# Kernel tuning notes

Hardware: AMD Instinct MI355X
Metric: run time of the kernel (lower is better)

## Reference

```python
import jax, jax.numpy as jnp
import numpy as np

N_NODES = 10000
N_EDGES = 80000
N_GRAPHS = 64
H, D = 4, 512          # num_heads, out_feats
EMB = 768
HFEAT = 512
NCLS = 2
SLOPE = 0.2            # DGL GATConv default negative_slope
BN_EPS = 1e-5


def setup_inputs() -> dict:
    key = jax.random.key(0)
    ks = jax.random.split(key, 24)
    f32 = jnp.float32
    rn = lambda k, s, sc=0.02: jax.random.normal(k, s, dtype=f32) * sc
    inp = {
        "node_feat": jax.random.normal(ks[0], (N_NODES, EMB), dtype=f32),
        "func_feat": jax.random.normal(ks[1], (N_NODES, EMB), dtype=f32),
        "W1": rn(ks[2], (EMB, H * D)),
        "al1": rn(ks[3], (H, D), 0.1),
        "ar1": rn(ks[4], (H, D), 0.1),
        "b1": jnp.zeros((H * D,), f32),
        "W2": rn(ks[5], (H * D, H * D)),
        "al2": rn(ks[6], (H, D), 0.1),
        "ar2": rn(ks[7], (H, D), 0.1),
        "b2": jnp.zeros((H * D,), f32),
        "Wfc": rn(ks[8], (H * D, HFEAT)),
        "bfc": jnp.zeros((HFEAT,), f32),
        "Wfco": rn(ks[9], (EMB, HFEAT)),
        "bfco": jnp.zeros((HFEAT,), f32),
        "Wh": rn(ks[10], (8, HFEAT, HFEAT)),
        "bh": jnp.zeros((8, HFEAT), f32),
        "gamma": jnp.ones((HFEAT,), f32),
        "beta": jnp.zeros((HFEAT,), f32),
        "Whfc": rn(ks[11], (HFEAT, HFEAT)),
        "bhfc": jnp.zeros((HFEAT,), f32),
        "Wf": rn(ks[12], (HFEAT, NCLS)),
        "bf": jnp.zeros((NCLS,), f32),
        "src": jax.random.randint(ks[13], (N_EDGES,), 0, N_NODES),
        "dst": jax.random.randint(ks[14], (N_EDGES,), 0, N_NODES),
        "graph_id": jnp.sort(jax.random.randint(ks[15], (N_NODES,), 0, N_GRAPHS)),
    }
    return inp


def gat_conv(h, W, al, ar, b, src, dst):
    """DGL GATConv (eval mode): fc -> per-head attention logits -> edge
    softmax over incoming edges -> scatter-sum -> +bias. Returns (N, H*D)."""
    feat = (h @ W).reshape(-1, H, D)                      # (N,H,D)
    el = jnp.einsum('nhd,hd->nh', feat, al)               # (N,H)
    er = jnp.einsum('nhd,hd->nh', feat, ar)
    e = jax.nn.leaky_relu(el[src] + er[dst], SLOPE)       # (E,H)
    emax = jax.ops.segment_max(e, dst, num_segments=N_NODES)
    ex = jnp.exp(e - emax[dst])
    den = jax.ops.segment_sum(ex, dst, num_segments=N_NODES)
    a = ex / den[dst]                                     # edge softmax (E,H)
    msg = feat[src] * a[:, :, None]                       # (E,H,D) gather+weight
    out = jax.ops.segment_sum(msg, dst, num_segments=N_NODES)
    return (out + b.reshape(1, H, D)).reshape(-1, H * D)


def reference(node_feat, func_feat, W1, al1, ar1, b1, W2, al2, ar2, b2,
              Wfc, bfc, Wfco, bfco, Wh, bh, gamma, beta, Whfc, bhfc,
              Wf, bf, src, dst, graph_id):
    h = gat_conv(node_feat, W1, al1, ar1, b1, src, dst)   # (N, 2048)
    h = gat_conv(h, W2, al2, ar2, b2, src, dst)           # (N, 2048)
    h = jax.nn.elu(h @ Wfc + bfc)                         # (N, 512)
    h_func = jax.nn.elu(func_feat @ Wfco + bfco)          # (N, 512)
    for i in range(8):
        h = jax.nn.elu(h @ Wh[i] + bh[i])
        h_func = jax.nn.elu(h_func @ Wh[i] + bh[i])       # dead for output (as in torch)
    counts = jax.ops.segment_sum(jnp.ones((N_NODES,), h.dtype), graph_id,
                                 num_segments=N_GRAPHS)
    hg = jax.ops.segment_sum(h, graph_id, num_segments=N_GRAPHS)
    hg = hg / jnp.maximum(counts, 1.0)[:, None]           # dgl.mean_nodes (G, 512)
    # BatchNorm1d eval with running_mean=0, running_var=1
    hg = hg / jnp.sqrt(1.0 + BN_EPS) * gamma + beta
    hg = jax.nn.elu(hg @ Whfc + bhfc)
    return hg @ Wf + bf                                   # (G, NCLS)
```

## Files before the change

### kernel.cpp

```cpp
#include <hip/hip_runtime.h>
#include <hip/hip_bf16.h>
#include <math.h>

#define N_NODES 10000
#define N_EDGES 80000
#define N_GRAPHS 64
#define NH 4
#define HD 512
#define HDTOT 2048
#define EMB 768
#define HFEAT 512

typedef _Float16 half8 __attribute__((ext_vector_type(8)));
typedef _Float16 half4 __attribute__((ext_vector_type(4)));
typedef float f32x4 __attribute__((ext_vector_type(4)));

__device__ __forceinline__ void gload_lds16(const void* g, void* l) {
  __builtin_amdgcn_global_load_lds(
      (const __attribute__((address_space(1))) unsigned int*)g,
      (__attribute__((address_space(3))) unsigned int*)l, 16, 0, 0);
}

template <int BM>
__global__ __launch_bounds__(256) void gemm_f16_kernel(
    const _Float16* __restrict__ A, const _Float16* __restrict__ BT,
    const float* __restrict__ bias, _Float16* __restrict__ C,
    int M, int N, int K, int act) {
  constexpr int WR = (BM == 128) ? 2 : 1;
  constexpr int WC = 4 / WR;
  constexpr int MI = (BM / WR) / 16;
  constexpr int NI = (128 / WC) / 16;
  constexpr int NW = NI * 16;
  constexpr int CS = NW + 4;
  constexpr int GPR = NW / 8;

  __shared__ _Float16 smem[(BM + 128) * 32];
  _Float16* As = smem;
  _Float16* Bs = smem + BM * 32;

  const int bn = blockIdx.x * 128, bm = blockIdx.y * BM;
  const int t = threadIdx.x;
  const int lane = t & 63, wave = t >> 6;
  const int wr = wave / WC, wc = wave % WC;
  const int m0 = wr * (BM / WR), n0 = wc * NW;
  const int fr = lane & 15, fq = lane >> 4;

  f32x4 acc[MI][NI];
#pragma unroll
  for (int i = 0; i < MI; ++i)
#pragma unroll
    for (int j = 0; j < NI; ++j) acc[i][j] = (f32x4){0.f, 0.f, 0.f, 0.f};

  for (int k0 = 0; k0 < K; k0 += 32) {
    __syncthreads();
#pragma unroll
    for (int it = 0; it < BM / 64; ++it) {
      int gid = it * 256 + t;
      int r = gid >> 2;
      int q = (gid & 3) ^ ((r >> 1) & 3);
      int grow = bm + r;
      if (grow >= M) grow = M - 1;
      gload_lds16(A + (size_t)grow * K + k0 + q * 8,
                  &As[(it * 256 + wave * 64) * 8]);
    }
#pragma unroll
    for (int it = 0; it < 2; ++it) {
      int gid = it * 256 + t;
      int r = gid >> 2;
      int q = (gid & 3) ^ ((r >> 1) & 3);
      gload_lds16(BT + (size_t)(bn + r) * K + k0 + q * 8,
                  &Bs[(it * 256 + wave * 64) * 8]);
    }
    __syncthreads();

    half8 af[MI], bf[NI];
#pragma unroll
    for (int mi = 0; mi < MI; ++mi) {
      int m = m0 + mi * 16 + fr;
      af[mi] = *(const half8*)&As[m * 32 + (fq ^ ((m >> 1) & 3)) * 8];
    }
#pragma unroll
    for (int ni = 0; ni < NI; ++ni) {
      int n = n0 + ni * 16 + fr;
      bf[ni] = *(const half8*)&Bs[n * 32 + (fq ^ ((n >> 1) & 3)) * 8];
    }
#pragma unroll
    for (int mi = 0; mi < MI; ++mi)
#pragma unroll
      for (int ni = 0; ni < NI; ++ni)
        acc[mi][ni] = __builtin_amdgcn_mfma_f32_16x16x32_f16(
            af[mi], bf[ni], acc[mi][ni], 0, 0, 0);
  }
  __syncthreads();
  _Float16* cs = smem + wave * 16 * CS;
#pragma unroll
  for (int mi = 0; mi < MI; ++mi) {
#pragma unroll
    for (int ni = 0; ni < NI; ++ni) {
      float bb = bias ? bias[bn + n0 + ni * 16 + fr] : 0.f;
#pragma unroll
      for (int j = 0; j < 4; ++j) {
        float v = acc[mi][ni][j] + bb;
        if (act == 1) v = v > 0.f ? v : expm1f(v);
        cs[(fq * 4 + j) * CS + ni * 16 + fr] = (_Float16)v;
      }
    }
#pragma unroll
    for (int i = 0; i < NW / 32; ++i) {
      int piece = i * 64 + lane;
      int r = piece / GPR, g = piece % GPR;
      int grow = bm + m0 + mi * 16 + r;
      if (grow < M) {
        half8 v = *(const half8*)&cs[r * CS + g * 8];
        *(half8*)&C[(size_t)grow * N + bn + n0 + g * 8] = v;
      }
    }
  }
}

__global__ __launch_bounds__(256) void convert_wt_kernel(
    const float* __restrict__ W, _Float16* __restrict__ WT, int K, int N) {
  __shared__ float tile[32][33];
  W += (size_t)blockIdx.z * K * N;
  WT += (size_t)blockIdx.z * K * N;
  int k0 = blockIdx.x * 32, n0 = blockIdx.y * 32;
  int t = threadIdx.x;
  int r = t >> 3, c4 = (t & 7) * 4;
  float4 v = *(const float4*)(W + (size_t)(k0 + r) * N + n0 + c4);
  tile[r][c4 + 0] = v.x;
  tile[r][c4 + 1] = v.y;
  tile[r][c4 + 2] = v.z;
  tile[r][c4 + 3] = v.w;
  __syncthreads();
  float x0 = tile[c4 + 0][r], x1 = tile[c4 + 1][r];
  float x2 = tile[c4 + 2][r], x3 = tile[c4 + 3][r];
  size_t o = (size_t)(n0 + r) * K + k0 + c4;
  *(half4*)&WT[o] = (half4){(_Float16)x0, (_Float16)x1, (_Float16)x2, (_Float16)x3};
}

__global__ void convert_f32_f16_kernel(const float* __restrict__ x,
                                       _Float16* __restrict__ y, int n4) {
  int gid = blockIdx.x * blockDim.x + threadIdx.x;
  if (gid >= n4) return;
  float4 v = *(const float4*)(x + gid * 4);
  *(half4*)(y + gid * 4) =
      (half4){(_Float16)v.x, (_Float16)v.y, (_Float16)v.z, (_Float16)v.w};
}

__global__ void hist_kernel(const int* __restrict__ dst, int* __restrict__ cnt, int E) {
  int gid = blockIdx.x * blockDim.x + threadIdx.x;
  if (gid < E) atomicAdd(&cnt[dst[gid]], 1);
}

__global__ void scan_kernel(const int* __restrict__ cnt, int* __restrict__ row_ptr,
                            int* __restrict__ cursor, int n) {
  __shared__ int part[256];
  int t = threadIdx.x;
  int chunk = (n + 255) / 256;
  int s0 = t * chunk;
  int s1 = min(s0 + chunk, n);
  int sum = 0;
  for (int i = s0; i < s1; ++i) sum += cnt[i];
  part[t] = sum;
  __syncthreads();
  if (t == 0) {
    int acc = 0;
    for (int i = 0; i < 256; ++i) { int v = part[i]; part[i] = acc; acc += v; }
    row_ptr[n] = acc;
  }
  __syncthreads();
  int run = part[t];
  for (int i = s0; i < s1; ++i) {
    row_ptr[i] = run;
    cursor[i] = run;
    run += cnt[i];
  }
}

__global__ void scatter_kernel(const int* __restrict__ src, const int* __restrict__ dst,
                               int* __restrict__ cursor, int* __restrict__ csr_src,
                               int* __restrict__ csr_dst, int E) {
  int gid = blockIdx.x * blockDim.x + threadIdx.x;
  if (gid < E) {
    int d = dst[gid];
    int pos = atomicAdd(&cursor[d], 1);
    csr_src[pos] = src[gid];
    csr_dst[pos] = d;
  }
}

__global__ __launch_bounds__(256) void el_er_kernel(
    const _Float16* __restrict__ feat, const float* __restrict__ al,
    const float* __restrict__ ar, float* __restrict__ el, float* __restrict__ er) {
  int n = blockIdx.x;
  int t = threadIdx.x;
  int h = t >> 6, lane = t & 63;
  half8 f = *(const half8*)(feat + (size_t)n * HDTOT + h * HD + lane * 8);
  const float* ap = al + h * HD + lane * 8;
  const float* rp = ar + h * HD + lane * 8;
  float4 a0 = *(const float4*)ap, a1 = *(const float4*)(ap + 4);
  float4 r0 = *(const float4*)rp, r1 = *(const float4*)(rp + 4);
  float f0 = (float)f[0], f1 = (float)f[1], f2 = (float)f[2], f3 = (float)f[3];
  float f4 = (float)f[4], f5 = (float)f[5], f6 = (float)f[6], f7 = (float)f[7];
  float sl = f0 * a0.x + f1 * a0.y + f2 * a0.z + f3 * a0.w +
             f4 * a1.x + f5 * a1.y + f6 * a1.z + f7 * a1.w;
  float sr = f0 * r0.x + f1 * r0.y + f2 * r0.z + f3 * r0.w +
             f4 * r1.x + f5 * r1.y + f6 * r1.z + f7 * r1.w;
  for (int off = 32; off; off >>= 1) {
    sl += __shfl_down(sl, off);
    sr += __shfl_down(sr, off);
  }
  if (lane == 0) {
    el[n * NH + h] = sl;
    er[n * NH + h] = sr;
  }
}

__global__ void edge_e_kernel(const float* __restrict__ el, const float* __restrict__ er,
                              const int* __restrict__ csr_src,
                              const int* __restrict__ csr_dst,
                              float* __restrict__ e_buf, int EH) {
  int gid = blockIdx.x * blockDim.x + threadIdx.x;
  if (gid >= EH) return;
  int p = gid >> 2, h = gid & 3;
  float v = el[csr_src[p] * NH + h] + er[csr_dst[p] * NH + h];
  e_buf[gid] = v >= 0.f ? v : 0.2f * v;
}

__global__ __launch_bounds__(256) void node_softmax_kernel(
    float* __restrict__ e_buf, const int* __restrict__ row_ptr,
    float* __restrict__ den) {
  int n = blockIdx.x;
  int t = threadIdx.x;
  int h = t >> 6, lane = t & 63;
  int s = row_ptr[n], epos = row_ptr[n + 1];
  if (s == epos) return;
  float m = -INFINITY;
  for (int p = s + lane; p < epos; p += 64) m = fmaxf(m, e_buf[p * NH + h]);
  for (int off = 32; off; off >>= 1) m = fmaxf(m, __shfl_xor(m, off));
  float sum = 0.f;
  for (int p = s + lane; p < epos; p += 64) {
    float ex = expf(e_buf[p * NH + h] - m);
    e_buf[p * NH + h] = ex;
    sum += ex;
  }
  for (int off = 32; off; off >>= 1) sum += __shfl_xor(sum, off);
  if (lane == 0) den[n * NH + h] = sum;
}

__global__ __launch_bounds__(256) void aggregate_kernel(
    const _Float16* __restrict__ feat, const float* __restrict__ e_buf,
    const float* __restrict__ den, const int* __restrict__ row_ptr,
    const int* __restrict__ csr_src, const float* __restrict__ bias,
    _Float16* __restrict__ out) {
  int n = blockIdx.x;
  int t = threadIdx.x;
  int base = t * 8;
  int h = t >> 6;
  float acc[8] = {0.f, 0.f, 0.f, 0.f, 0.f, 0.f, 0.f, 0.f};
  int s = row_ptr[n], epos = row_ptr[n + 1];
  float inv_den = 0.f;
  if (s < epos) inv_den = 1.f / den[n * NH + h];
  int p = s;
  for (; p + 4 <= epos; p += 4) {
    int sn0 = csr_src[p + 0], sn1 = csr_src[p + 1];
    int sn2 = csr_src[p + 2], sn3 = csr_src[p + 3];
    float a0 = e_buf[(p + 0) * NH + h] * inv_den;
    float a1 = e_buf[(p + 1) * NH + h] * inv_den;
    float a2 = e_buf[(p + 2) * NH + h] * inv_den;
    float a3 = e_buf[(p + 3) * NH + h] * inv_den;
    half8 f0 = *(const half8*)(feat + (size_t)sn0 * HDTOT + base);
    half8 f1 = *(const half8*)(feat + (size_t)sn1 * HDTOT + base);
    half8 f2 = *(const half8*)(feat + (size_t)sn2 * HDTOT + base);
    half8 f3 = *(const half8*)(feat + (size_t)sn3 * HDTOT + base);
#pragma unroll
    for (int i = 0; i < 8; ++i)
      acc[i] += a0 * (float)f0[i] + a1 * (float)f1[i] +
                a2 * (float)f2[i] + a3 * (float)f3[i];
  }
  for (; p < epos; ++p) {
    int sn = csr_src[p];
    float a = e_buf[p * NH + h] * inv_den;
    half8 f = *(const half8*)(feat + (size_t)sn * HDTOT + base);
#pragma unroll
    for (int i = 0; i < 8; ++i) acc[i] += a * (float)f[i];
  }
  float4 b0 = *(const float4*)(bias + base);
  float4 b1 = *(const float4*)(bias + base + 4);
  half8 o;
  o[0] = (_Float16)(acc[0] + b0.x); o[1] = (_Float16)(acc[1] + b0.y);
  o[2] = (_Float16)(acc[2] + b0.z); o[3] = (_Float16)(acc[3] + b0.w);
  o[4] = (_Float16)(acc[4] + b1.x); o[5] = (_Float16)(acc[5] + b1.y);
  o[6] = (_Float16)(acc[6] + b1.z); o[7] = (_Float16)(acc[7] + b1.w);
  *(half8*)(out + (size_t)n * HDTOT + base) = o;
}

__global__ __launch_bounds__(512) void pool_kernel(
    const _Float16* __restrict__ h, const int* __restrict__ graph_id,
    float* __restrict__ hg, float* __restrict__ counts) {
  int g = blockIdx.x;
  __shared__ int s_lo, s_hi;
  if (threadIdx.x == 0) {
    int lo = 0, hi = N_NODES;
    while (lo < hi) { int m = (lo + hi) >> 1; if (graph_id[m] < g) lo = m + 1; else hi = m; }
    s_lo = lo;
    int lo2 = lo, hi2 = N_NODES;
    while (lo2 < hi2) { int m = (lo2 + hi2) >> 1; if (graph_id[m] < g + 1) lo2 = m + 1; else hi2 = m; }
    s_hi = lo2;
  }
  __syncthreads();
  int lo = s_lo, hi = s_hi;
  int col = threadIdx.x;
  float acc = 0.f;
  for (int n = lo; n < hi; ++n) acc += (float)h[(size_t)n * HFEAT + col];
  hg[g * HFEAT + col] = acc;
  if (col == 0) counts[g] = (float)(hi - lo);
}

__global__ __launch_bounds__(256) void final_kernel(
    const float* __restrict__ hg, const float* __restrict__ counts,
    const float* __restrict__ gamma, const float* __restrict__ beta,
    const float* __restrict__ Whfc, const float* __restrict__ bhfc,
    const float* __restrict__ Wf, const float* __restrict__ bf,
    float* __restrict__ out) {
  __shared__ float sh[HFEAT];
  __shared__ float st[HFEAT];
  __shared__ float r0[4], r1[4];
  int g = blockIdx.x, t = threadIdx.x;
  float invc = 1.f / fmaxf(counts[g], 1.f);
  float bnscale = rsqrtf(1.f + 1e-5f);
  for (int j = t; j < HFEAT; j += 256) {
    float v = hg[g * HFEAT + j] * invc;
    sh[j] = v * bnscale * gamma[j] + beta[j];
  }
  __syncthreads();
  for (int j = t; j < HFEAT; j += 256) {
    float acc = bhfc[j];
    for (int k = 0; k < HFEAT; ++k) acc += sh[k] * Whfc[k * HFEAT + j];
    st[j] = acc > 0.f ? acc : expm1f(acc);
  }
  __syncthreads();
  float p0 = 0.f, p1 = 0.f;
  for (int j = t; j < HFEAT; j += 256) {
    p0 += st[j] * Wf[j * 2 + 0];
    p1 += st[j] * Wf[j * 2 + 1];
  }
  for (int off = 32; off; off >>= 1) {
    p0 += __shfl_down(p0, off);
    p1 += __shfl_down(p1, off);
  }
  int w = t >> 6;
  if ((t & 63) == 0) { r0[w] = p0; r1[w] = p1; }
  __syncthreads();
  if (t == 0) {
    out[g * 2 + 0] = r0[0] + r0[1] + r0[2] + r0[3] + bf[0];
    out[g * 2 + 1] = r1[0] + r1[1] + r1[2] + r1[3] + bf[1];
  }
}

static void gemm_raw(const _Float16* A, const _Float16* wt, const float* bias,
                     _Float16* C, int M, int N, int K, int act,
                     bool small_m_tile, hipStream_t stream) {
  if (small_m_tile) {
    dim3 grid(N / 128, (M + 63) / 64);
    hipLaunchKernelGGL(gemm_f16_kernel<64>, grid, dim3(256), 0, stream,
                       A, wt, bias, C, M, N, K, act);
  } else {
    dim3 grid(N / 128, (M + 127) / 128);
    hipLaunchKernelGGL(gemm_f16_kernel<128>, grid, dim3(256), 0, stream,
                       A, wt, bias, C, M, N, K, act);
  }
}

static void gemm(const _Float16* A, const float* W, _Float16* wt,
                 const float* bias, _Float16* C, int M, int N, int K, int act,
                 bool small_m_tile, hipStream_t stream) {
  hipLaunchKernelGGL(convert_wt_kernel, dim3(K / 32, N / 32, 1), dim3(256),
                     0, stream, W, wt, K, N);
  gemm_raw(A, wt, bias, C, M, N, K, act, small_m_tile, stream);
}

static void gat_layer(const _Float16* h_in, int K_in, const float* W, _Float16* wt,
                      const float* al, const float* ar, const float* b,
                      const int* row_ptr, const int* csr_src, const int* csr_dst,
                      _Float16* featbuf, float* el, float* er,
                      float* e_buf, float* den, _Float16* out, hipStream_t stream) {
  gemm(h_in, W, wt, nullptr, featbuf, N_NODES, HDTOT, K_in, 0, false, stream);
  hipLaunchKernelGGL(el_er_kernel, dim3(N_NODES), dim3(256), 0, stream, featbuf, al, ar, el, er);
  int EH = N_EDGES * NH;
  hipLaunchKernelGGL(edge_e_kernel, dim3((EH + 255) / 256), dim3(256), 0, stream,
                     el, er, csr_src, csr_dst, e_buf, EH);
  hipLaunchKernelGGL(node_softmax_kernel, dim3(N_NODES), dim3(256), 0, stream,
                     e_buf, row_ptr, den);
  hipLaunchKernelGGL(aggregate_kernel, dim3(N_NODES), dim3(256), 0, stream,
                     featbuf, e_buf, den, row_ptr, csr_src, b, out);
}

extern "C" void kernel_launch(void* const* d_in, const int* in_sizes, int n_in,
                              void* d_out, int out_size, void* d_ws, size_t ws_size,
                              hipStream_t stream) {
  const float* node_feat = (const float*)d_in[0];
  const float* W1 = (const float*)d_in[2];
  const float* al1 = (const float*)d_in[3];
  const float* ar1 = (const float*)d_in[4];
  const float* b1 = (const float*)d_in[5];
  const float* W2 = (const float*)d_in[6];
  const float* al2 = (const float*)d_in[7];
  const float* ar2 = (const float*)d_in[8];
  const float* b2 = (const float*)d_in[9];
  const float* Wfc = (const float*)d_in[10];
  const float* bfc = (const float*)d_in[11];
  const float* Wh = (const float*)d_in[14];
  const float* bh = (const float*)d_in[15];
  const float* gamma = (const float*)d_in[16];
  const float* beta = (const float*)d_in[17];
  const float* Whfc = (const float*)d_in[18];
  const float* bhfc = (const float*)d_in[19];
  const float* Wf = (const float*)d_in[20];
  const float* bf = (const float*)d_in[21];
  const int* src = (const int*)d_in[22];
  const int* dst = (const int*)d_in[23];
  const int* graph_id = (const int*)d_in[24];
  float* out = (float*)d_out;

  _Float16* P0 = (_Float16*)d_ws;
  _Float16* P1 = P0 + (size_t)N_NODES * HDTOT;
  _Float16* Pin = P1 + (size_t)N_NODES * HDTOT;
  _Float16* wt = Pin + (size_t)N_NODES * EMB;
  _Float16* whh = wt + (size_t)2048 * 2048;
  float* el = (float*)(whh + (size_t)8 * HFEAT * HFEAT);
  float* er = el + N_NODES * NH;
  float* e_buf = er + N_NODES * NH;
  float* den = e_buf + (size_t)N_EDGES * NH;
  float* hg = den + N_NODES * NH;
  float* counts = hg + N_GRAPHS * HFEAT;
  int* cnt = (int*)(counts + N_GRAPHS);
  int* row_ptr = cnt + N_NODES;
  int* cursor = row_ptr + N_NODES + 1;
  int* csr_src = cursor + N_NODES;
  int* csr_dst = csr_src + N_EDGES;

  hipMemsetAsync(cnt, 0, N_NODES * sizeof(int), stream);
  hipLaunchKernelGGL(hist_kernel, dim3((N_EDGES + 255) / 256), dim3(256), 0, stream,
                     dst, cnt, N_EDGES);
  hipLaunchKernelGGL(scan_kernel, dim3(1), dim3(256), 0, stream, cnt, row_ptr, cursor, N_NODES);
  hipLaunchKernelGGL(scatter_kernel, dim3((N_EDGES + 255) / 256), dim3(256), 0, stream,
                     src, dst, cursor, csr_src, csr_dst, N_EDGES);

  int n4 = N_NODES * EMB / 4;
  hipLaunchKernelGGL(convert_f32_f16_kernel, dim3((n4 + 255) / 256), dim3(256), 0, stream,
                     node_feat, Pin, n4);
  hipLaunchKernelGGL(convert_wt_kernel, dim3(HFEAT / 32, HFEAT / 32, 8),
                     dim3(256), 0, stream, Wh, whh, HFEAT, HFEAT);

  gat_layer(Pin, EMB, W1, wt, al1, ar1, b1, row_ptr, csr_src, csr_dst,
            P0, el, er, e_buf, den, P1, stream);
  gat_layer(P1, HDTOT, W2, wt, al2, ar2, b2, row_ptr, csr_src, csr_dst,
            P0, el, er, e_buf, den, P1, stream);

  gemm(P1, Wfc, wt, bfc, P0, N_NODES, HFEAT, HDTOT, 1, true, stream);

  _Float16* cur = P0;
  _Float16* nxt = P1;
  for (int i = 0; i < 8; ++i) {
    gemm_raw(cur, whh + (size_t)i * HFEAT * HFEAT, bh + (size_t)i * HFEAT, nxt,
             N_NODES, HFEAT, HFEAT, 1, true, stream);
    _Float16* tmp = cur; cur = nxt; nxt = tmp;
  }

  hipLaunchKernelGGL(pool_kernel, dim3(N_GRAPHS), dim3(512), 0, stream,
                     cur, graph_id, hg, counts);

  hipLaunchKernelGGL(final_kernel, dim3(N_GRAPHS), dim3(256), 0, stream,
                     hg, counts, gamma, beta, Whfc, bhfc, Wf, bf, out);
}
```

Measured before the change: 816.9 us.

## Double GEMM K-tile to 64 and fuse edge logits into edge softmax

The GEMM main loop now stages 64-wide K slices per iteration, using an 8-way XOR swizzle and two MFMA sub-steps. This halves the number of barrier pairs and load rounds, at the cost of doubling LDS per block. The separate edge-logit kernel is folded into a per-node edge softmax kernel that computes leaky-relu logits from el[src] plus a hoisted er[n], then normalizes in place. That removes the csr_dst array, the den buffer and the divide in aggregation, but adds an extra pass over e_buf inside the softmax kernel.

Measured after the change: 763.6 us. 1.07x faster.

```diff
diff --git a/kernel.cpp b/kernel.cpp
--- a/kernel.cpp
+++ b/kernel.cpp
@@ -34,9 +34,9 @@
   constexpr int CS = NW + 4;
   constexpr int GPR = NW / 8;
 
-  __shared__ _Float16 smem[(BM + 128) * 32];
+  __shared__ _Float16 smem[(BM + 128) * 64];
   _Float16* As = smem;
-  _Float16* Bs = smem + BM * 32;
+  _Float16* Bs = smem + BM * 64;
 
   const int bn = blockIdx.x * 128, bm = blockIdx.y * BM;
   const int t = threadIdx.x;
@@ -51,45 +51,48 @@
 #pragma unroll
     for (int j = 0; j < NI; ++j) acc[i][j] = (f32x4){0.f, 0.f, 0.f, 0.f};
 
-  for (int k0 = 0; k0 < K; k0 += 32) {
+  for (int k0 = 0; k0 < K; k0 += 64) {
     __syncthreads();
 #pragma unroll
-    for (int it = 0; it < BM / 64; ++it) {
+    for (int it = 0; it < BM / 32; ++it) {
       int gid = it * 256 + t;
-      int r = gid >> 2;
-      int q = (gid & 3) ^ ((r >> 1) & 3);
+      int r = gid >> 3;
+      int q = (gid & 7) ^ (r & 7);
       int grow = bm + r;
       if (grow >= M) grow = M - 1;
       gload_lds16(A + (size_t)grow * K + k0 + q * 8,
                   &As[(it * 256 + wave * 64) * 8]);
     }
 #pragma unroll
-    for (int it = 0; it < 2; ++it) {
+    for (int it = 0; it < 4; ++it) {
       int gid = it * 256 + t;
-      int r = gid >> 2;
-      int q = (gid & 3) ^ ((r >> 1) & 3);
+      int r = gid >> 3;
+      int q = (gid & 7) ^ (r & 7);
       gload_lds16(BT + (size_t)(bn + r) * K + k0 + q * 8,
                   &Bs[(it * 256 + wave * 64) * 8]);
     }
     __syncthreads();
 
-    half8 af[MI], bf[NI];
-#pragma unroll
-    for (int mi = 0; mi < MI; ++mi) {
-      int m = m0 + mi * 16 + fr;
-      af[mi] = *(const half8*)&As[m * 32 + (fq ^ ((m >> 1) & 3)) * 8];
+#pragma unroll
+    for (int kk = 0; kk < 2; ++kk) {
+      half8 af[MI], bf[NI];
+#pragma unroll
+      for (int mi = 0; mi < MI; ++mi) {
+        int m = m0 + mi * 16 + fr;
+        af[mi] = *(const half8*)&As[m * 64 + (((kk * 4 + fq) ^ (m & 7))) * 8];
+      }
+#pragma unroll
+      for (int ni = 0; ni < NI; ++ni) {
+        int n = n0 + ni * 16 + fr;
+        bf[ni] = *(const half8*)&Bs[n * 64 + (((kk * 4 + fq) ^ (n & 7))) * 8];
+      }
+#pragma unroll
+      for (int mi = 0; mi < MI; ++mi)
+#pragma unroll
+        for (int ni = 0; ni < NI; ++ni)
+          acc[mi][ni] = __builtin_amdgcn_mfma_f32_16x16x32_f16(
+              af[mi], bf[ni], acc[mi][ni], 0, 0, 0);
     }
-#pragma unroll
-    for (int ni = 0; ni < NI; ++ni) {
-      int n = n0 + ni * 16 + fr;
-      bf[ni] = *(const half8*)&Bs[n * 32 + (fq ^ ((n >> 1) & 3)) * 8];
-    }
-#pragma unroll
-    for (int mi = 0; mi < MI; ++mi)
-#pragma unroll
-      for (int ni = 0; ni < NI; ++ni)
-        acc[mi][ni] = __builtin_amdgcn_mfma_f32_16x16x32_f16(
-            af[mi], bf[ni], acc[mi][ni], 0, 0, 0);
   }
   __syncthreads();
   _Float16* cs = smem + wave * 16 * CS;
@@ -179,13 +182,12 @@
 
 __global__ void scatter_kernel(const int* __restrict__ src, const int* __restrict__ dst,
                                int* __restrict__ cursor, int* __restrict__ csr_src,
-                               int* __restrict__ csr_dst, int E) {
+                               int E) {
   int gid = blockIdx.x * blockDim.x + threadIdx.x;
   if (gid < E) {
     int d = dst[gid];
     int pos = atomicAdd(&cursor[d], 1);
     csr_src[pos] = src[gid];
-    csr_dst[pos] = d;
   }
 }
 
@@ -216,27 +218,23 @@
   }
 }
 
-__global__ void edge_e_kernel(const float* __restrict__ el, const float* __restrict__ er,
-                              const int* __restrict__ csr_src,
-                              const int* __restrict__ csr_dst,
-                              float* __restrict__ e_buf, int EH) {
-  int gid = blockIdx.x * blockDim.x + threadIdx.x;
-  if (gid >= EH) return;
-  int p = gid >> 2, h = gid & 3;
-  float v = el[csr_src[p] * NH + h] + er[csr_dst[p] * NH + h];
-  e_buf[gid] = v >= 0.f ? v : 0.2f * v;
-}
-
-__global__ __launch_bounds__(256) void node_softmax_kernel(
-    float* __restrict__ e_buf, const int* __restrict__ row_ptr,
-    float* __restrict__ den) {
+__global__ __launch_bounds__(256) void edge_softmax_kernel(
+    const float* __restrict__ el, const float* __restrict__ er,
+    const int* __restrict__ csr_src, const int* __restrict__ row_ptr,
+    float* __restrict__ e_buf) {
   int n = blockIdx.x;
   int t = threadIdx.x;
   int h = t >> 6, lane = t & 63;
   int s = row_ptr[n], epos = row_ptr[n + 1];
   if (s == epos) return;
+  float ern = er[n * NH + h];
   float m = -INFINITY;
-  for (int p = s + lane; p < epos; p += 64) m = fmaxf(m, e_buf[p * NH + h]);
+  for (int p = s + lane; p < epos; p += 64) {
+    float v = el[csr_src[p] * NH + h] + ern;
+    v = v >= 0.f ? v : 0.2f * v;
+    e_buf[p * NH + h] = v;
+    m = fmaxf(m, v);
+  }
   for (int off = 32; off; off >>= 1) m = fmaxf(m, __shfl_xor(m, off));
   float sum = 0.f;
   for (int p = s + lane; p < epos; p += 64) {
@@ -245,30 +243,28 @@
     sum += ex;
   }
   for (int off = 32; off; off >>= 1) sum += __shfl_xor(sum, off);
-  if (lane == 0) den[n * NH + h] = sum;
+  float inv = 1.f / sum;
+  for (int p = s + lane; p < epos; p += 64) e_buf[p * NH + h] *= inv;
 }
 
 __global__ __launch_bounds__(256) void aggregate_kernel(
     const _Float16* __restrict__ feat, const float* __restrict__ e_buf,
-    const float* __restrict__ den, const int* __restrict__ row_ptr,
-    const int* __restrict__ csr_src, const float* __restrict__ bias,
-    _Float16* __restrict__ out) {
+    const int* __restrict__ row_ptr, const int* __restrict__ csr_src,
+    const float* __restrict__ bias, _Float16* __restrict__ out) {
   int n = blockIdx.x;
   int t = threadIdx.x;
   int base = t * 8;
   int h = t >> 6;
   float acc[8] = {0.f, 0.f, 0.f, 0.f, 0.f, 0.f, 0.f, 0.f};
   int s = row_ptr[n], epos = row_ptr[n + 1];
-  float inv_den = 0.f;
-  if (s < epos) inv_den = 1.f / den[n * NH + h];
   int p = s;
   for (; p + 4 <= epos; p += 4) {
     int sn0 = csr_src[p + 0], sn1 = csr_src[p + 1];
     int sn2 = csr_src[p + 2], sn3 = csr_src[p + 3];
-    float a0 = e_buf[(p + 0) * NH + h] * inv_den;
-    float a1 = e_buf[(p + 1) * NH + h] * inv_den;
-    float a2 = e_buf[(p + 2) * NH + h] * inv_den;
-    float a3 = e_buf[(p + 3) * NH + h] * inv_den;
+    float a0 = e_buf[(p + 0) * NH + h];
+    float a1 = e_buf[(p + 1) * NH + h];
+    float a2 = e_buf[(p + 2) * NH + h];
+    float a3 = e_buf[(p + 3) * NH + h];
     half8 f0 = *(const half8*)(feat + (size_t)sn0 * HDTOT + base);
     half8 f1 = *(const half8*)(feat + (size_t)sn1 * HDTOT + base);
     half8 f2 = *(const half8*)(feat + (size_t)sn2 * HDTOT + base);
@@ -280,7 +276,7 @@
   }
   for (; p < epos; ++p) {
     int sn = csr_src[p];
-    float a = e_buf[p * NH + h] * inv_den;
+    float a = e_buf[p * NH + h];
     half8 f = *(const half8*)(feat + (size_t)sn * HDTOT + base);
 #pragma unroll
     for (int i = 0; i < 8; ++i) acc[i] += a * (float)f[i];
@@ -382,18 +378,15 @@
 
 static void gat_layer(const _Float16* h_in, int K_in, const float* W, _Float16* wt,
                       const float* al, const float* ar, const float* b,
-                      const int* row_ptr, const int* csr_src, const int* csr_dst,
+                      const int* row_ptr, const int* csr_src,
                       _Float16* featbuf, float* el, float* er,
-                      float* e_buf, float* den, _Float16* out, hipStream_t stream) {
+                      float* e_buf, _Float16* out, hipStream_t stream) {
   gemm(h_in, W, wt, nullptr, featbuf, N_NODES, HDTOT, K_in, 0, false, stream);
   hipLaunchKernelGGL(el_er_kernel, dim3(N_NODES), dim3(256), 0, stream, featbuf, al, ar, el, er);
-  int EH = N_EDGES * NH;
-  hipLaunchKernelGGL(edge_e_kernel, dim3((EH + 255) / 256), dim3(256), 0, stream,
-                     el, er, csr_src, csr_dst, e_buf, EH);
-  hipLaunchKernelGGL(node_softmax_kernel, dim3(N_NODES), dim3(256), 0, stream,
-                     e_buf, row_ptr, den);
+  hipLaunchKernelGGL(edge_softmax_kernel, dim3(N_NODES), dim3(256), 0, stream,
+                     el, er, csr_src, row_ptr, e_buf);
   hipLaunchKernelGGL(aggregate_kernel, dim3(N_NODES), dim3(256), 0, stream,
-                     featbuf, e_buf, den, row_ptr, csr_src, b, out);
+                     featbuf, e_buf, row_ptr, csr_src, b, out);
 }
 
 extern "C" void kernel_launch(void* const* d_in, const int* in_sizes, int n_in,
@@ -431,21 +424,19 @@
   float* el = (float*)(whh + (size_t)8 * HFEAT * HFEAT);
   float* er = el + N_NODES * NH;
   float* e_buf = er + N_NODES * NH;
-  float* den = e_buf + (size_t)N_EDGES * NH;
-  float* hg = den + N_NODES * NH;
+  float* hg = e_buf + (size_t)N_EDGES * NH;
   float* counts = hg + N_GRAPHS * HFEAT;
   int* cnt = (int*)(counts + N_GRAPHS);
   int* row_ptr = cnt + N_NODES;
   int* cursor = row_ptr + N_NODES + 1;
   int* csr_src = cursor + N_NODES;
-  int* csr_dst = csr_src + N_EDGES;
 
   hipMemsetAsync(cnt, 0, N_NODES * sizeof(int), stream);
   hipLaunchKernelGGL(hist_kernel, dim3((N_EDGES + 255) / 256), dim3(256), 0, stream,
                      dst, cnt, N_EDGES);
   hipLaunchKernelGGL(scan_kernel, dim3(1), dim3(256), 0, stream, cnt, row_ptr, cursor, N_NODES);
   hipLaunchKernelGGL(scatter_kernel, dim3((N_EDGES + 255) / 256), dim3(256), 0, stream,
-                     src, dst, cursor, csr_src, csr_dst, N_EDGES);
+                     src, dst, cursor, csr_src, N_EDGES);
 
   int n4 = N_NODES * EMB / 4;
   hipLaunchKernelGGL(convert_f32_f16_kernel, dim3((n4 + 255) / 256), dim3(256), 0, stream,
@@ -453,10 +444,10 @@
   hipLaunchKernelGGL(convert_wt_kernel, dim3(HFEAT / 32, HFEAT / 32, 8),
                      dim3(256), 0, stream, Wh, whh, HFEAT, HFEAT);
 
-  gat_layer(Pin, EMB, W1, wt, al1, ar1, b1, row_ptr, csr_src, csr_dst,
-            P0, el, er, e_buf, den, P1, stream);
-  gat_layer(P1, HDTOT, W2, wt, al2, ar2, b2, row_ptr, csr_src, csr_dst,
-            P0, el, er, e_buf, den, P1, stream);
+  gat_layer(Pin, EMB, W1, wt, al1, ar1, b1, row_ptr, csr_src,
+            P0, el, er, e_buf, P1, stream);
+  gat_layer(P1, HDTOT, W2, wt, al2, ar2, b2, row_ptr, csr_src,
+            P0, el, er, e_buf, P1, stream);
 
   gemm(P1, Wfc, wt, bfc, P0, N_NODES, HFEAT, HDTOT, 1, true, stream);
 
```
